# Kernel tuning notes

Hardware: AMD Instinct MI355X
Metric: run time of the kernel (lower is better)

## Reference

```python
import jax, jax.numpy as jnp
import numpy as np

N = 100000   # nodes
E = 3200000  # edges (avg degree 32)
F = 128      # num_features
H = 256      # hidden_dim
D = 256      # embedding_dim
O = 2        # output_dim
BN_EPS = 1e-5


def _mk_layer(keys, fin, fmid, fout):
    kW1, kW2 = keys
    W1 = jax.random.normal(kW1, (fin, fmid), jnp.float32) / np.sqrt(fin)
    b1 = jnp.zeros((fmid,), jnp.float32)
    g = jnp.ones((fmid,), jnp.float32)
    be = jnp.zeros((fmid,), jnp.float32)
    mu = jnp.zeros((fmid,), jnp.float32)
    var = jnp.ones((fmid,), jnp.float32)
    W2 = jax.random.normal(kW2, (fmid, fout), jnp.float32) / np.sqrt(fmid)
    b2 = jnp.zeros((fout,), jnp.float32)
    return W1, b1, g, be, mu, var, W2, b2


def setup_inputs() -> dict:
    key = jax.random.key(0)
    ks = jax.random.split(key, 10)
    inp = {}
    inp["x"] = jax.random.normal(ks[0], (N, F), jnp.float32)
    inp["edge_index"] = jax.random.randint(ks[1], (2, E), 0, N, jnp.int32)
    names = ["W1", "b1", "g", "be", "mu", "var", "W2", "b2"]
    for pref, (fin, fmid, fout), kk in [
        ("l1", (F, H, H), (ks[2], ks[3])),
        ("l2", (H, H, H), (ks[4], ks[5])),
        ("l3", (H, H, D), (ks[6], ks[7])),
    ]:
        vals = _mk_layer(kk, fin, fmid, fout)
        for n, v in zip(names, vals):
            inp[f"{pref}_{n}"] = v
    inp["out_W"] = jax.random.normal(ks[8], (D, O), jnp.float32) / np.sqrt(D)
    inp["out_b"] = jnp.zeros((O,), jnp.float32)
    return inp


def gin_layer(h, src, dst, W1, b1, g, be, mu, var, W2, b2, final_relu):
    # GINConv (eps=0): z_i = x_i + sum_{j->i} x_j, then MLP(Linear-BN-ReLU-Linear[-ReLU])
    agg = jax.ops.segment_sum(h[src], dst, num_segments=N)
    z = h + agg
    z = z @ W1 + b1
    z = (z - mu) * jax.lax.rsqrt(var + BN_EPS) * g + be  # BatchNorm1d (inference)
    z = jax.nn.relu(z)
    z = z @ W2 + b2
    if final_relu:
        z = jax.nn.relu(z)
    return z


def reference(x, edge_index,
              l1_W1, l1_b1, l1_g, l1_be, l1_mu, l1_var, l1_W2, l1_b2,
              l2_W1, l2_b1, l2_g, l2_be, l2_mu, l2_var, l2_W2, l2_b2,
              l3_W1, l3_b1, l3_g, l3_be, l3_mu, l3_var, l3_W2, l3_b2,
              out_W, out_b):
    src, dst = edge_index[0], edge_index[1]
    h = gin_layer(x, src, dst, l1_W1, l1_b1, l1_g, l1_be, l1_mu, l1_var, l1_W2, l1_b2, True)
    h = gin_layer(h, src, dst, l2_W1, l2_b1, l2_g, l2_be, l2_mu, l2_var, l2_W2, l2_b2, True)
    h = gin_layer(h, src, dst, l3_W1, l3_b1, l3_g, l3_be, l3_mu, l3_var, l3_W2, l3_b2, False)
    return h @ out_W + out_b  # [N, O]
```

## Files before the change

### kernel.cpp

```cpp
#include <hip/hip_runtime.h>
#include <cstdint>
#include <cstddef>

#define N_NODES 100000
#define N_EDGES 3200000
#define MPAD    100096
#define HID     256
#define NBUCK   196
#define BSH     9
#define BSTRIDE 18432

typedef _Float16 f16;
typedef _Float16 f16x2 __attribute__((ext_vector_type(2)));
typedef _Float16 f16x8 __attribute__((ext_vector_type(8)));
typedef float    f32x4 __attribute__((ext_vector_type(4)));
typedef float    f32x2 __attribute__((ext_vector_type(2)));

union F16x2 { unsigned u; f16 h[2]; f16x2 v; };
__device__ inline void unpack2(unsigned u, float& a, float& b) {
    F16x2 x; x.u = u; a = (float)x.h[0]; b = (float)x.h[1];
}
__device__ inline unsigned pack2(float a, float b) {
    F16x2 x; x.h[0] = (f16)a; x.h[1] = (f16)b; return x.u;
}

__global__ __launch_bounds__(256) void k_bucketA(const int* __restrict__ src,
                                                 const int* __restrict__ dst,
                                                 unsigned* __restrict__ pairs,
                                                 int* __restrict__ nb, int e) {
    __shared__ int hist[NBUCK];
    __shared__ int lbase[NBUCK];
    __shared__ int lcur[NBUCK];
    const int t = threadIdx.x;
    for (int i = t; i < NBUCK; i += 256) hist[i] = 0;
    __syncthreads();
    const int e0 = blockIdx.x * 4096;
    bool v[16]; int d[16], s[16];
#pragma unroll
    for (int i = 0; i < 16; ++i) {
        int idx = e0 + i * 256 + t;
        v[i] = idx < e;
        d[i] = v[i] ? dst[idx] : 0;
        s[i] = v[i] ? src[idx] : 0;
    }
#pragma unroll
    for (int i = 0; i < 16; ++i)
        if (v[i]) atomicAdd(&hist[d[i] >> BSH], 1);
    __syncthreads();
    for (int i = t; i < NBUCK; i += 256) {
        int h = hist[i];
        lbase[i] = h ? atomicAdd(&nb[i], h) : 0;
        lcur[i] = 0;
    }
    __syncthreads();
#pragma unroll
    for (int i = 0; i < 16; ++i) {
        if (v[i]) {
            int b = d[i] >> BSH;
            int p = atomicAdd(&lcur[b], 1);
            unsigned packed = ((unsigned)(d[i] & 511) << 17) | (unsigned)s[i];
            pairs[(size_t)b * BSTRIDE + lbase[b] + p] = packed;
        }
    }
}

__global__ void k_scan196(const int* __restrict__ nb, int* __restrict__ bbase,
                          int* __restrict__ rowptrN) {
    __shared__ int s[256];
    int t = threadIdx.x;
    int v = (t < NBUCK) ? nb[t] : 0;
    s[t] = v;
    __syncthreads();
    for (int off = 1; off < 256; off <<= 1) {
        int u = (t >= off) ? s[t - off] : 0;
        __syncthreads();
        s[t] += u;
        __syncthreads();
    }
    if (t < NBUCK) bbase[t] = s[t] - v;
    if (t == 0) *rowptrN = N_EDGES;
}

__global__ __launch_bounds__(256) void k_bucketB(const unsigned* __restrict__ pairs,
                                                 const int* __restrict__ nb,
                                                 const int* __restrict__ bbase,
                                                 int* __restrict__ rowptr,
                                                 int* __restrict__ colidx) {
    __shared__ int deg[512];
    __shared__ int sc[512];
    __shared__ int cur[512];
    const int b = blockIdx.x, t = threadIdx.x;
    const int cnt = nb[b], base = bbase[b];
    const unsigned* P = pairs + (size_t)b * BSTRIDE;
    deg[t] = 0; deg[t + 256] = 0;
    __syncthreads();
    for (int i = t; i < cnt; i += 256) atomicAdd(&deg[P[i] >> 17], 1);
    __syncthreads();
    sc[t] = deg[t]; sc[t + 256] = deg[t + 256];
    __syncthreads();
    for (int off = 1; off < 512; off <<= 1) {
        int a0 = (t >= off) ? sc[t - off] : 0;
        int a1 = (t + 256 >= off) ? sc[t + 256 - off] : 0;
        __syncthreads();
        sc[t] += a0; sc[t + 256] += a1;
        __syncthreads();
    }
    int node0 = b << BSH;
#pragma unroll
    for (int rep = 0; rep < 2; ++rep) {
        int i = t + rep * 256;
        int excl = base + sc[i] - deg[i];
        cur[i] = excl;
        int node = node0 + i;
        if (node < N_NODES) rowptr[node] = excl;
    }
    __syncthreads();
    for (int i = t; i < cnt; i += 256) {
        unsigned p = P[i];
        int pos = atomicAdd(&cur[p >> 17], 1);
        colidx[pos] = (int)(p & 0x1FFFF) << 6;
    }
}

__global__ void k_cvt8(const float2* __restrict__ x, unsigned short* __restrict__ o, int n) {
    int t = blockIdx.x * 256 + threadIdx.x;
    if (t < n) {
        float2 v = x[t];
        int pk = __builtin_amdgcn_cvt_pk_fp8_f32(v.x, v.y, 0, false);
        o[t] = (unsigned short)(pk & 0xffff);
    }
}

__global__ void k_foldw1(const float* __restrict__ W, const float* __restrict__ b1,
                         const float* __restrict__ gm, const float* __restrict__ bt,
                         const float* __restrict__ mu, const float* __restrict__ vr,
                         f16* __restrict__ Wt, float* __restrict__ bias, int K) {
    int t = blockIdx.x * 256 + threadIdx.x;
    if (t >= K * 256) return;
    int n = t & 255, k = t >> 8;
    float sc = gm[n] * rsqrtf(vr[n] + 1e-5f);
    Wt[n * K + k] = (f16)(W[t] * sc);
    if (k == 0) bias[n] = (b1[n] - mu[n]) * sc + bt[n];
}

__global__ void k_transb(const float* __restrict__ W, f16* __restrict__ Wt) {
    int t = blockIdx.x * 256 + threadIdx.x;
    int n = t & 255, k = t >> 8;
    Wt[n * 256 + k] = (f16)W[t];
}

__global__ void k_fold2(const float* __restrict__ W2, const float* __restrict__ b2,
                        const float* __restrict__ outW, const float* __restrict__ outb,
                        float* __restrict__ W2o, float* __restrict__ bo) {
    int k = threadIdx.x;
    float a0 = 0.f, a1 = 0.f;
    for (int j = 0; j < 256; ++j) {
        float w = W2[k * 256 + j];
        a0 += w * outW[j * 2 + 0];
        a1 += w * outW[j * 2 + 1];
    }
    W2o[k * 2 + 0] = a0;
    W2o[k * 2 + 1] = a1;
    if (k < 2) {
        float b = outb[k];
        for (int j = 0; j < 256; ++j) b += b2[j] * outW[j * 2 + k];
        bo[k] = b;
    }
}

__global__ void k_agg256(const unsigned* __restrict__ h8,
                         const int* __restrict__ rp, const int* __restrict__ ci,
                         uint2* __restrict__ z, int n) {
    int gw = (blockIdx.x * 256 + threadIdx.x) >> 6;
    if (gw >= n) return;
    int lane = threadIdx.x & 63;
    const unsigned* h8l = h8 + lane;
    f32x2 A01, A23;
    {
        unsigned u = h8l[(size_t)gw * 64];
        A01 = __builtin_amdgcn_cvt_pk_f32_fp8(u, false);
        A23 = __builtin_amdgcn_cvt_pk_f32_fp8(u, true);
    }
    int s = rp[gw], e = rp[gw + 1];
    int p = s;
    for (; p + 7 < e; p += 8) {
        int j0 = ci[p],     j1 = ci[p + 1], j2 = ci[p + 2], j3 = ci[p + 3];
        int j4 = ci[p + 4], j5 = ci[p + 5], j6 = ci[p + 6], j7 = ci[p + 7];
        unsigned u0 = h8l[(size_t)j0], u1 = h8l[(size_t)j1];
        unsigned u2 = h8l[(size_t)j2], u3 = h8l[(size_t)j3];
        unsigned u4 = h8l[(size_t)j4], u5 = h8l[(size_t)j5];
        unsigned u6 = h8l[(size_t)j6], u7 = h8l[(size_t)j7];
#pragma unroll
        for (int q = 0; q < 8; ++q) {
            unsigned u = q == 0 ? u0 : q == 1 ? u1 : q == 2 ? u2 : q == 3 ? u3
                       : q == 4 ? u4 : q == 5 ? u5 : q == 6 ? u6 : u7;
            A01 += __builtin_amdgcn_cvt_pk_f32_fp8(u, false);
            A23 += __builtin_amdgcn_cvt_pk_f32_fp8(u, true);
        }
    }
    for (; p < e; ++p) {
        unsigned u = h8l[(size_t)ci[p]];
        A01 += __builtin_amdgcn_cvt_pk_f32_fp8(u, false);
        A23 += __builtin_amdgcn_cvt_pk_f32_fp8(u, true);
    }
    uint2 o; o.x = pack2(A01[0], A01[1]); o.y = pack2(A23[0], A23[1]);
    z[(size_t)gw * 64 + lane] = o;
}

__global__ void k_agg128(const unsigned short* __restrict__ x8,
                         const int* __restrict__ rp, const int* __restrict__ ci,
                         unsigned* __restrict__ z, int n) {
    int gw = (blockIdx.x * 256 + threadIdx.x) >> 6;
    if (gw >= n) return;
    int lane = threadIdx.x & 63;
    const unsigned short* xl = x8 + lane;
    f32x2 A01 = __builtin_amdgcn_cvt_pk_f32_fp8((unsigned)xl[(size_t)gw * 64], false);
    int s = rp[gw], e = rp[gw + 1];
    int p = s;
    for (; p + 7 < e; p += 8) {
        int j0 = ci[p],     j1 = ci[p + 1], j2 = ci[p + 2], j3 = ci[p + 3];
        int j4 = ci[p + 4], j5 = ci[p + 5], j6 = ci[p + 6], j7 = ci[p + 7];
        unsigned u0 = xl[(size_t)j0], u1 = xl[(size_t)j1];
        unsigned u2 = xl[(size_t)j2], u3 = xl[(size_t)j3];
        unsigned u4 = xl[(size_t)j4], u5 = xl[(size_t)j5];
        unsigned u6 = xl[(size_t)j6], u7 = xl[(size_t)j7];
        A01 += __builtin_amdgcn_cvt_pk_f32_fp8(u0, false);
        A01 += __builtin_amdgcn_cvt_pk_f32_fp8(u1, false);
        A01 += __builtin_amdgcn_cvt_pk_f32_fp8(u2, false);
        A01 += __builtin_amdgcn_cvt_pk_f32_fp8(u3, false);
        A01 += __builtin_amdgcn_cvt_pk_f32_fp8(u4, false);
        A01 += __builtin_amdgcn_cvt_pk_f32_fp8(u5, false);
        A01 += __builtin_amdgcn_cvt_pk_f32_fp8(u6, false);
        A01 += __builtin_amdgcn_cvt_pk_f32_fp8(u7, false);
    }
    for (; p < e; ++p)
        A01 += __builtin_amdgcn_cvt_pk_f32_fp8((unsigned)xl[(size_t)ci[p]], false);
    z[(size_t)gw * 64 + lane] = pack2(A01[0], A01[1]);
}

template <int K, bool RELU, bool ST16, bool ST8>
__global__ __launch_bounds__(256, 2) void k_gemm2(const f16* __restrict__ A,
                                                  const f16* __restrict__ Bt,
                                                  const float* __restrict__ bias,
                                                  f16* __restrict__ C,
                                                  unsigned char* __restrict__ C8) {
    __shared__ f16 As[128 * 64];
    __shared__ f16 Bs[256 * 64];
    const int tid = threadIdx.x;
    const int bm0 = blockIdx.x * 128;
    const int lane = tid & 63, wave = tid >> 6;
    const int quad = lane >> 4, l16 = lane & 15;
    const int wr = (wave >> 1) * 64;
    const int wc = (wave & 1) * 128;
    f32x4 acc[4][8] = {};
    const f16* Abase = A + (size_t)bm0 * K;

    for (int k0 = 0; k0 < K; k0 += 64) {
#pragma unroll
        for (int i = 0; i < 4; ++i) {
            int c = i * 256 + tid;
            int m = c >> 3;
            int gg = (c & 7) ^ (m & 7);
            __builtin_amdgcn_global_load_lds(
                (const __attribute__((address_space(1))) unsigned int*)(Abase + (size_t)m * K + k0 + gg * 8),
                (__attribute__((address_space(3))) unsigned int*)(As + (size_t)c * 8), 16, 0, 0);
        }
#pragma unroll
        for (int i = 0; i < 8; ++i) {
            int c = i * 256 + tid;
            int m = c >> 3;
            int gg = (c & 7) ^ (m & 7);
            __builtin_amdgcn_global_load_lds(
                (const __attribute__((address_space(1))) unsigned int*)(Bt + (size_t)m * K + k0 + gg * 8),
                (__attribute__((address_space(3))) unsigned int*)(Bs + (size_t)c * 8), 16, 0, 0);
        }
        __syncthreads();
#pragma unroll
        for (int kk = 0; kk < 64; kk += 32) {
            const int gbase = kk >> 3;
            f16x8 af[4], bfv[8];
#pragma unroll
            for (int mi = 0; mi < 4; ++mi) {
                int m = wr + mi * 16 + l16;
                int slot = (gbase + quad) ^ (m & 7);
                af[mi] = *(const f16x8*)&As[(m * 8 + slot) * 8];
            }
#pragma unroll
            for (int ni = 0; ni < 8; ++ni) {
                int m = wc + ni * 16 + l16;
                int slot = (gbase + quad) ^ (m & 7);
                bfv[ni] = *(const f16x8*)&Bs[(m * 8 + slot) * 8];
            }
#pragma unroll
            for (int mi = 0; mi < 4; ++mi)
#pragma unroll
                for (int ni = 0; ni < 8; ++ni)
                    acc[mi][ni] = __builtin_amdgcn_mfma_f32_16x16x32_f16(af[mi], bfv[ni], acc[mi][ni], 0, 0, 0);
        }
        __syncthreads();
    }

    float bv[8];
#pragma unroll
    for (int ni = 0; ni < 8; ++ni) bv[ni] = bias[wc + ni * 16 + l16];
#pragma unroll
    for (int mi = 0; mi < 4; ++mi) {
#pragma unroll
        for (int r = 0; r < 4; ++r) {
            size_t row = (size_t)(bm0 + wr + mi * 16 + quad * 4 + r);
#pragma unroll
            for (int ni = 0; ni < 8; ++ni) {
                float v = acc[mi][ni][r] + bv[ni];
                if (RELU) v = fmaxf(v, 0.f);
                int col = wc + ni * 16 + l16;
                if (ST16) C[row * HID + col] = (f16)v;
                if (ST8) {
                    int pk = __builtin_amdgcn_cvt_pk_fp8_f32(v, v, 0, false);
                    C8[row * HID + col] = (unsigned char)(pk & 0xff);
                }
            }
        }
    }
}

__global__ void k_head(const uint2* __restrict__ y, const float* __restrict__ W2o,
                       const float* __restrict__ bo, float* __restrict__ out, int n) {
    __shared__ float w[512];
    __shared__ float bb[2];
    int t = threadIdx.x;
    w[t] = W2o[t];
    w[t + 256] = W2o[t + 256];
    if (t < 2) bb[t] = bo[t];
    __syncthreads();
    int gw = (blockIdx.x * 256 + t) >> 6;
    if (gw >= n) return;
    int lane = t & 63;
    uint2 d = y[(size_t)gw * 64 + lane];
    float x0, x1, x2, x3;
    unpack2(d.x, x0, x1); unpack2(d.y, x2, x3);
    int k = lane * 4;
    float o0 = x0 * w[k * 2 + 0] + x1 * w[k * 2 + 2] + x2 * w[k * 2 + 4] + x3 * w[k * 2 + 6];
    float o1 = x0 * w[k * 2 + 1] + x1 * w[k * 2 + 3] + x2 * w[k * 2 + 5] + x3 * w[k * 2 + 7];
#pragma unroll
    for (int off = 32; off > 0; off >>= 1) {
        o0 += __shfl_down(o0, off);
        o1 += __shfl_down(o1, off);
    }
    if (lane == 0) {
        out[(size_t)gw * 2 + 0] = o0 + bb[0];
        out[(size_t)gw * 2 + 1] = o1 + bb[1];
    }
}

extern "C" void kernel_launch(void* const* d_in, const int* in_sizes, int n_in,
                              void* d_out, int out_size, void* d_ws, size_t ws_size,
                              hipStream_t stream) {
    const float* x    = (const float*)d_in[0];
    const int*   ei   = (const int*)d_in[1];
    const int*   esrc = ei;
    const int*   edst = ei + N_EDGES;
    const float* lw[3][8];
    for (int l = 0; l < 3; ++l)
        for (int j = 0; j < 8; ++j) lw[l][j] = (const float*)d_in[2 + l * 8 + j];
    const float* outW = (const float*)d_in[26];
    const float* outB = (const float*)d_in[27];

    char* base = (char*)d_ws;
    size_t off = 0;
    auto alloc = [&](size_t bytes) -> void* {
        void* r = base + off;
        off += (bytes + 255) & ~(size_t)255;
        return r;
    };
    f16* z  = (f16*)alloc((size_t)MPAD * 256 * 2);
    f16* y  = (f16*)alloc((size_t)MPAD * 256 * 2);
    unsigned char* h8 = (unsigned char*)alloc((size_t)MPAD * 256);
    unsigned short* x8 = (unsigned short*)alloc((size_t)MPAD * 64 * 2);
    f16* W1t[3]; float* bias1[3]; f16* W2t[2];
    W1t[0] = (f16*)alloc(256 * 128 * 2);
    W1t[1] = (f16*)alloc(256 * 256 * 2);
    W1t[2] = (f16*)alloc(256 * 256 * 2);
    for (int l = 0; l < 2; ++l) W2t[l] = (f16*)alloc(256 * 256 * 2);
    for (int l = 0; l < 3; ++l) bias1[l] = (float*)alloc(256 * 4);
    float* W2o = (float*)alloc(512 * 4);
    float* bo  = (float*)alloc(2 * 4);
    unsigned* pairs = (unsigned*)alloc((size_t)NBUCK * BSTRIDE * 4);
    int* nb     = (int*)alloc(NBUCK * 4);
    int* bbase  = (int*)alloc(NBUCK * 4);
    int* rowptr = (int*)alloc((size_t)(N_NODES + 1) * 4);
    int* colidx = (int*)alloc((size_t)N_EDGES * 4);

    hipMemsetAsync(nb, 0, NBUCK * 4, stream);
    k_bucketA<<<(N_EDGES + 4095) / 4096, 256, 0, stream>>>(esrc, edst, pairs, nb, N_EDGES);
    k_scan196<<<1, 256, 0, stream>>>(nb, bbase, rowptr + N_NODES);
    k_bucketB<<<NBUCK, 256, 0, stream>>>(pairs, nb, bbase, rowptr, colidx);

    k_cvt8<<<(N_NODES * 64 + 255) / 256, 256, 0, stream>>>((const float2*)x, x8, N_NODES * 64);
    k_foldw1<<<128, 256, 0, stream>>>(lw[0][0], lw[0][1], lw[0][2], lw[0][3], lw[0][4], lw[0][5], W1t[0], bias1[0], 128);
    k_foldw1<<<256, 256, 0, stream>>>(lw[1][0], lw[1][1], lw[1][2], lw[1][3], lw[1][4], lw[1][5], W1t[1], bias1[1], 256);
    k_foldw1<<<256, 256, 0, stream>>>(lw[2][0], lw[2][1], lw[2][2], lw[2][3], lw[2][4], lw[2][5], W1t[2], bias1[2], 256);
    k_transb<<<256, 256, 0, stream>>>(lw[0][6], W2t[0]);
    k_transb<<<256, 256, 0, stream>>>(lw[1][6], W2t[1]);
    k_fold2<<<1, 256, 0, stream>>>(lw[2][6], lw[2][7], outW, outB, W2o, bo);

    const int GG = MPAD / 128;
    const int WBLOCKS = (N_NODES + 3) / 4;

    k_agg128<<<WBLOCKS, 256, 0, stream>>>(x8, rowptr, colidx, (unsigned*)z, N_NODES);
    k_gemm2<128, true, true,  false><<<GG, 256, 0, stream>>>(z, W1t[0], bias1[0], y, nullptr);
    k_gemm2<256, true, false, true ><<<GG, 256, 0, stream>>>(y, W2t[0], lw[0][7], nullptr, h8);
    k_agg256<<<WBLOCKS, 256, 0, stream>>>((const unsigned*)h8, rowptr, colidx, (uint2*)z, N_NODES);
    k_gemm2<256, true, true,  false><<<GG, 256, 0, stream>>>(z, W1t[1], bias1[1], y, nullptr);
    k_gemm2<256, true, false, true ><<<GG, 256, 0, stream>>>(y, W2t[1], lw[1][7], nullptr, h8);
    k_agg256<<<WBLOCKS, 256, 0, stream>>>((const unsigned*)h8, rowptr, colidx, (uint2*)z, N_NODES);
    k_gemm2<256, true, true,  false><<<GG, 256, 0, stream>>>(z, W1t[2], bias1[2], y, nullptr);
    k_head<<<WBLOCKS, 256, 0, stream>>>((const uint2*)y, W2o, bo, (float*)d_out, N_NODES);
}
```

Before: 719.6 us.

## Fuse both MLP GEMMs per layer with FP8 second GEMM and fused output head

```diff
diff --git a/kernel.cpp b/kernel.cpp
--- a/kernel.cpp
+++ b/kernel.cpp
@@ -15,13 +15,14 @@
 typedef _Float16 f16x8 __attribute__((ext_vector_type(8)));
 typedef float    f32x4 __attribute__((ext_vector_type(4)));
 typedef float    f32x2 __attribute__((ext_vector_type(2)));
+typedef long long i64;
 
 union F16x2 { unsigned u; f16 h[2]; f16x2 v; };
+__device__ inline unsigned pack2(float a, float b) {
+    F16x2 x; x.h[0] = (f16)a; x.h[1] = (f16)b; return x.u;
+}
 __device__ inline void unpack2(unsigned u, float& a, float& b) {
     F16x2 x; x.u = u; a = (float)x.h[0]; b = (float)x.h[1];
-}
-__device__ inline unsigned pack2(float a, float b) {
-    F16x2 x; x.h[0] = (f16)a; x.h[1] = (f16)b; return x.u;
 }
 
 __global__ __launch_bounds__(256) void k_bucketA(const int* __restrict__ src,
@@ -143,10 +144,12 @@
     if (k == 0) bias[n] = (b1[n] - mu[n]) * sc + bt[n];
 }
 
-__global__ void k_transb(const float* __restrict__ W, f16* __restrict__ Wt) {
+__global__ void k_transb8(const float* __restrict__ W, unsigned char* __restrict__ W8) {
     int t = blockIdx.x * 256 + threadIdx.x;
     int n = t & 255, k = t >> 8;
-    Wt[n * 256 + k] = (f16)W[t];
+    float v = W[t];
+    int pk = __builtin_amdgcn_cvt_pk_fp8_f32(v, v, 0, false);
+    W8[n * 256 + k] = (unsigned char)(pk & 0xff);
 }
 
 __global__ void k_fold2(const float* __restrict__ W2, const float* __restrict__ b2,
@@ -238,31 +241,178 @@
     z[(size_t)gw * 64 + lane] = pack2(A01[0], A01[1]);
 }
 
-template <int K, bool RELU, bool ST16, bool ST8>
-__global__ __launch_bounds__(256, 2) void k_gemm2(const f16* __restrict__ A,
-                                                  const f16* __restrict__ Bt,
-                                                  const float* __restrict__ bias,
-                                                  f16* __restrict__ C,
-                                                  unsigned char* __restrict__ C8) {
+template <int K>
+__global__ __launch_bounds__(256, 2) void k_layer(const f16* __restrict__ A,
+                                                  const f16* __restrict__ W1,
+                                                  const float* __restrict__ b1,
+                                                  const unsigned char* __restrict__ W28,
+                                                  const float* __restrict__ b2,
+                                                  unsigned char* __restrict__ H8) {
     __shared__ f16 As[128 * 64];
     __shared__ f16 Bs[256 * 64];
+    __shared__ unsigned char Ys[128 * 256];
     const int tid = threadIdx.x;
     const int bm0 = blockIdx.x * 128;
     const int lane = tid & 63, wave = tid >> 6;
     const int quad = lane >> 4, l16 = lane & 15;
     const int wr = (wave >> 1) * 64;
     const int wc = (wave & 1) * 128;
+    const f16* Abase = A + (size_t)bm0 * K;
+
+    {
+        f32x4 acc[4][8] = {};
+        for (int k0 = 0; k0 < K; k0 += 64) {
+#pragma unroll
+            for (int i = 0; i < 4; ++i) {
+                int c = i * 256 + tid;
+                int m = c >> 3;
+                int gg = (c & 7) ^ (m & 7);
+                __builtin_amdgcn_global_load_lds(
+                    (const __attribute__((address_space(1))) unsigned int*)(Abase + (size_t)m * K + k0 + gg * 8),
+                    (__attribute__((address_space(3))) unsigned int*)(As + (size_t)c * 8), 16, 0, 0);
+            }
+#pragma unroll
+            for (int i = 0; i < 8; ++i) {
+                int c = i * 256 + tid;
+                int m = c >> 3;
+                int gg = (c & 7) ^ (m & 7);
+                __builtin_amdgcn_global_load_lds(
+                    (const __attribute__((address_space(1))) unsigned int*)(W1 + (size_t)m * K + k0 + gg * 8),
+                    (__attribute__((address_space(3))) unsigned int*)(Bs + (size_t)c * 8), 16, 0, 0);
+            }
+            __syncthreads();
+#pragma unroll
+            for (int kk = 0; kk < 64; kk += 32) {
+                const int gbase = kk >> 3;
+                f16x8 af[4], bfv[8];
+#pragma unroll
+                for (int mi = 0; mi < 4; ++mi) {
+                    int m = wr + mi * 16 + l16;
+                    int slot = (gbase + quad) ^ (m & 7);
+                    af[mi] = *(const f16x8*)&As[(m * 8 + slot) * 8];
+                }
+#pragma unroll
+                for (int ni = 0; ni < 8; ++ni) {
+                    int m = wc + ni * 16 + l16;
+                    int slot = (gbase + quad) ^ (m & 7);
+                    bfv[ni] = *(const f16x8*)&Bs[(m * 8 + slot) * 8];
+                }
+#pragma unroll
+                for (int mi = 0; mi < 4; ++mi)
+#pragma unroll
+                    for (int ni = 0; ni < 8; ++ni)
+                        acc[mi][ni] = __builtin_amdgcn_mfma_f32_16x16x32_f16(af[mi], bfv[ni], acc[mi][ni], 0, 0, 0);
+            }
+            __syncthreads();
+        }
+        float bv[8];
+#pragma unroll
+        for (int ni = 0; ni < 8; ++ni) bv[ni] = b1[wc + ni * 16 + l16];
+#pragma unroll
+        for (int mi = 0; mi < 4; ++mi) {
+#pragma unroll
+            for (int r = 0; r < 4; ++r) {
+                int row = wr + mi * 16 + quad * 4 + r;
+#pragma unroll
+                for (int ni = 0; ni < 8; ++ni) {
+                    float v = fmaxf(acc[mi][ni][r] + bv[ni], 0.f);
+                    int col = wc + ni * 16 + l16;
+                    int pk = __builtin_amdgcn_cvt_pk_fp8_f32(v, v, 0, false);
+                    int g = col >> 3, j = col & 7;
+                    Ys[row * 256 + ((g ^ (row & 15)) * 8 + j)] = (unsigned char)(pk & 0xff);
+                }
+            }
+        }
+    }
+    __syncthreads();
+
+    unsigned char* B8 = (unsigned char*)As;
+    f32x4 acc2[4][8] = {};
+    for (int k0 = 0; k0 < 256; k0 += 64) {
+#pragma unroll
+        for (int i = 0; i < 4; ++i) {
+            int c = i * 256 + tid;
+            int n = c >> 2;
+            int cg = c & 3;
+            int gg = cg ^ (n & 3);
+            __builtin_amdgcn_global_load_lds(
+                (const __attribute__((address_space(1))) unsigned int*)(W28 + (size_t)n * 256 + k0 + gg * 16),
+                (__attribute__((address_space(3))) unsigned int*)(B8 + (size_t)c * 16), 16, 0, 0);
+        }
+        __syncthreads();
+#pragma unroll
+        for (int kk = 0; kk < 64; kk += 32) {
+            int gq = (kk >> 3) + quad;
+            int gglob = ((k0 + kk) >> 3) + quad;
+            i64 af[4], bf[8];
+#pragma unroll
+            for (int mi = 0; mi < 4; ++mi) {
+                int m = wr + mi * 16 + l16;
+                af[mi] = *(const i64*)&Ys[m * 256 + ((gglob ^ (m & 15)) * 8)];
+            }
+#pragma unroll
+            for (int ni = 0; ni < 8; ++ni) {
+                int n = wc + ni * 16 + l16;
+                int cg2 = gq >> 1, sub = gq & 1;
+                bf[ni] = *(const i64*)&B8[n * 64 + (cg2 ^ (n & 3)) * 16 + sub * 8];
+            }
+#pragma unroll
+            for (int mi = 0; mi < 4; ++mi)
+#pragma unroll
+                for (int ni = 0; ni < 8; ++ni)
+                    acc2[mi][ni] = __builtin_amdgcn_mfma_f32_16x16x32_fp8_fp8(af[mi], bf[ni], acc2[mi][ni], 0, 0, 0);
+        }
+        __syncthreads();
+    }
+    float bv2[8];
+#pragma unroll
+    for (int ni = 0; ni < 8; ++ni) bv2[ni] = b2[wc + ni * 16 + l16];
+#pragma unroll
+    for (int mi = 0; mi < 4; ++mi) {
+#pragma unroll
+        for (int r = 0; r < 4; ++r) {
+            size_t row = (size_t)(bm0 + wr + mi * 16 + quad * 4 + r);
+#pragma unroll
+            for (int ni = 0; ni < 8; ++ni) {
+                float v = fmaxf(acc2[mi][ni][r] + bv2[ni], 0.f);
+                int col = wc + ni * 16 + l16;
+                int pk = __builtin_amdgcn_cvt_pk_fp8_f32(v, v, 0, false);
+                H8[row * HID + col] = (unsigned char)(pk & 0xff);
+            }
+        }
+    }
+}
+
+__global__ __launch_bounds__(256, 2) void k_layer3(const f16* __restrict__ A,
+                                                   const f16* __restrict__ W1,
+                                                   const float* __restrict__ b1,
+                                                   const float* __restrict__ W2o,
+                                                   const float* __restrict__ bo,
+                                                   float* __restrict__ out) {
+    __shared__ f16 As[128 * 64];
+    __shared__ f16 Bs[256 * 64];
+    __shared__ float W2s[512];
+    __shared__ float ob[256];
+    const int tid = threadIdx.x;
+    const int bm0 = blockIdx.x * 128;
+    const int lane = tid & 63, wave = tid >> 6;
+    const int quad = lane >> 4, l16 = lane & 15;
+    const int wr = (wave >> 1) * 64;
+    const int wc = (wave & 1) * 128;
+    const f16* Abase = A + (size_t)bm0 * 256;
+    W2s[tid] = W2o[tid];
+    W2s[tid + 256] = W2o[tid + 256];
+    ob[tid] = 0.f;
+
     f32x4 acc[4][8] = {};
-    const f16* Abase = A + (size_t)bm0 * K;
-
-    for (int k0 = 0; k0 < K; k0 += 64) {
+    for (int k0 = 0; k0 < 256; k0 += 64) {
 #pragma unroll
         for (int i = 0; i < 4; ++i) {
             int c = i * 256 + tid;
             int m = c >> 3;
             int gg = (c & 7) ^ (m & 7);
             __builtin_amdgcn_global_load_lds(
-                (const __attribute__((address_space(1))) unsigned int*)(Abase + (size_t)m * K + k0 + gg * 8),
+                (const __attribute__((address_space(1))) unsigned int*)(Abase + (size_t)m * 256 + k0 + gg * 8),
                 (__attribute__((address_space(3))) unsigned int*)(As + (size_t)c * 8), 16, 0, 0);
         }
 #pragma unroll
@@ -271,7 +421,7 @@
             int m = c >> 3;
             int gg = (c & 7) ^ (m & 7);
             __builtin_amdgcn_global_load_lds(
-                (const __attribute__((address_space(1))) unsigned int*)(Bt + (size_t)m * K + k0 + gg * 8),
+                (const __attribute__((address_space(1))) unsigned int*)(W1 + (size_t)m * 256 + k0 + gg * 8),
                 (__attribute__((address_space(3))) unsigned int*)(Bs + (size_t)c * 8), 16, 0, 0);
         }
         __syncthreads();
@@ -299,57 +449,37 @@
         }
         __syncthreads();
     }
-
     float bv[8];
 #pragma unroll
-    for (int ni = 0; ni < 8; ++ni) bv[ni] = bias[wc + ni * 16 + l16];
+    for (int ni = 0; ni < 8; ++ni) bv[ni] = b1[wc + ni * 16 + l16];
 #pragma unroll
     for (int mi = 0; mi < 4; ++mi) {
 #pragma unroll
         for (int r = 0; r < 4; ++r) {
-            size_t row = (size_t)(bm0 + wr + mi * 16 + quad * 4 + r);
+            int row = wr + mi * 16 + quad * 4 + r;
+            float p0 = 0.f, p1 = 0.f;
 #pragma unroll
             for (int ni = 0; ni < 8; ++ni) {
-                float v = acc[mi][ni][r] + bv[ni];
-                if (RELU) v = fmaxf(v, 0.f);
+                float v = fmaxf(acc[mi][ni][r] + bv[ni], 0.f);
                 int col = wc + ni * 16 + l16;
-                if (ST16) C[row * HID + col] = (f16)v;
-                if (ST8) {
-                    int pk = __builtin_amdgcn_cvt_pk_fp8_f32(v, v, 0, false);
-                    C8[row * HID + col] = (unsigned char)(pk & 0xff);
-                }
-            }
-        }
-    }
-}
-
-__global__ void k_head(const uint2* __restrict__ y, const float* __restrict__ W2o,
-                       const float* __restrict__ bo, float* __restrict__ out, int n) {
-    __shared__ float w[512];
-    __shared__ float bb[2];
-    int t = threadIdx.x;
-    w[t] = W2o[t];
-    w[t + 256] = W2o[t + 256];
-    if (t < 2) bb[t] = bo[t];
-    __syncthreads();
-    int gw = (blockIdx.x * 256 + t) >> 6;
-    if (gw >= n) return;
-    int lane = t & 63;
-    uint2 d = y[(size_t)gw * 64 + lane];
-    float x0, x1, x2, x3;
-    unpack2(d.x, x0, x1); unpack2(d.y, x2, x3);
-    int k = lane * 4;
-    float o0 = x0 * w[k * 2 + 0] + x1 * w[k * 2 + 2] + x2 * w[k * 2 + 4] + x3 * w[k * 2 + 6];
-    float o1 = x0 * w[k * 2 + 1] + x1 * w[k * 2 + 3] + x2 * w[k * 2 + 5] + x3 * w[k * 2 + 7];
-#pragma unroll
-    for (int off = 32; off > 0; off >>= 1) {
-        o0 += __shfl_down(o0, off);
-        o1 += __shfl_down(o1, off);
-    }
-    if (lane == 0) {
-        out[(size_t)gw * 2 + 0] = o0 + bb[0];
-        out[(size_t)gw * 2 + 1] = o1 + bb[1];
-    }
+                p0 += v * W2s[col * 2 + 0];
+                p1 += v * W2s[col * 2 + 1];
+            }
+#pragma unroll
+            for (int off = 1; off <= 8; off <<= 1) {
+                p0 += __shfl_xor(p0, off);
+                p1 += __shfl_xor(p1, off);
+            }
+            if (l16 == 0) {
+                atomicAdd(&ob[row * 2 + 0], p0);
+                atomicAdd(&ob[row * 2 + 1], p1);
+            }
+        }
+    }
+    __syncthreads();
+    int row = tid >> 1, o = tid & 1;
+    if (bm0 + row < N_NODES)
+        out[(size_t)(bm0 + row) * 2 + o] = ob[tid] + bo[o];
 }
 
 extern "C" void kernel_launch(void* const* d_in, const int* in_sizes, int n_in,
@@ -373,14 +503,13 @@
         return r;
     };
     f16* z  = (f16*)alloc((size_t)MPAD * 256 * 2);
-    f16* y  = (f16*)alloc((size_t)MPAD * 256 * 2);
     unsigned char* h8 = (unsigned char*)alloc((size_t)MPAD * 256);
     unsigned short* x8 = (unsigned short*)alloc((size_t)MPAD * 64 * 2);
-    f16* W1t[3]; float* bias1[3]; f16* W2t[2];
+    f16* W1t[3]; float* bias1[3]; unsigned char* W28[2];
     W1t[0] = (f16*)alloc(256 * 128 * 2);
     W1t[1] = (f16*)alloc(256 * 256 * 2);
     W1t[2] = (f16*)alloc(256 * 256 * 2);
-    for (int l = 0; l < 2; ++l) W2t[l] = (f16*)alloc(256 * 256 * 2);
+    for (int l = 0; l < 2; ++l) W28[l] = (unsigned char*)alloc(256 * 256);
     for (int l = 0; l < 3; ++l) bias1[l] = (float*)alloc(256 * 4);
     float* W2o = (float*)alloc(512 * 4);
     float* bo  = (float*)alloc(2 * 4);
@@ -399,20 +528,17 @@
     k_foldw1<<<128, 256, 0, stream>>>(lw[0][0], lw[0][1], lw[0][2], lw[0][3], lw[0][4], lw[0][5], W1t[0], bias1[0], 128);
     k_foldw1<<<256, 256, 0, stream>>>(lw[1][0], lw[1][1], lw[1][2], lw[1][3], lw[1][4], lw[1][5], W1t[1], bias1[1], 256);
     k_foldw1<<<256, 256, 0, stream>>>(lw[2][0], lw[2][1], lw[2][2], lw[2][3], lw[2][4], lw[2][5], W1t[2], bias1[2], 256);
-    k_transb<<<256, 256, 0, stream>>>(lw[0][6], W2t[0]);
-    k_transb<<<256, 256, 0, stream>>>(lw[1][6], W2t[1]);
+    k_transb8<<<256, 256, 0, stream>>>(lw[0][6], W28[0]);
+    k_transb8<<<256, 256, 0, stream>>>(lw[1][6], W28[1]);
     k_fold2<<<1, 256, 0, stream>>>(lw[2][6], lw[2][7], outW, outB, W2o, bo);
 
     const int GG = MPAD / 128;
     const int WBLOCKS = (N_NODES + 3) / 4;
 
     k_agg128<<<WBLOCKS, 256, 0, stream>>>(x8, rowptr, colidx, (unsigned*)z, N_NODES);
-    k_gemm2<128, true, true,  false><<<GG, 256, 0, stream>>>(z, W1t[0], bias1[0], y, nullptr);
-    k_gemm2<256, true, false, true ><<<GG, 256, 0, stream>>>(y, W2t[0], lw[0][7], nullptr, h8);
+    k_layer<128><<<GG, 256, 0, stream>>>(z, W1t[0], bias1[0], W28[0], lw[0][7], h8);
     k_agg256<<<WBLOCKS, 256, 0, stream>>>((const unsigned*)h8, rowptr, colidx, (uint2*)z, N_NODES);
-    k_gemm2<256, true, true,  false><<<GG, 256, 0, stream>>>(z, W1t[1], bias1[1], y, nullptr);
-    k_gemm2<256, true, false, true ><<<GG, 256, 0, stream>>>(y, W2t[1], lw[1][7], nullptr, h8);
+    k_layer<256><<<GG, 256, 0, stream>>>(z, W1t[1], bias1[1], W28[1], lw[1][7], h8);
     k_agg256<<<WBLOCKS, 256, 0, stream>>>((const unsigned*)h8, rowptr, colidx, (uint2*)z, N_NODES);
-    k_gemm2<256, true, true,  false><<<GG, 256, 0, stream>>>(z, W1t[2], bias1[2], y, nullptr);
-    k_head<<<WBLOCKS, 256, 0, stream>>>((const uint2*)y, W2o, bo, (float*)d_out, N_NODES);
-}
+    k_layer3<<<GG, 256, 0, stream>>>(z, W1t[2], bias1[2], W2o, bo, (float*)d_out);
+}
```

New measurement: 686.4 us. -4.6%, faster.
